# Optimization experiments

Measured on AMD Instinct MI355X. Metric: run time of the kernel, lower is better.

The kernel has to match this reference:

```python
import jax, jax.numpy as jnp
import numpy as np

OS_FACTOR = 2.0  # init kwarg; k = 1/os_factor Euler step size
B, T, IN, H = 32, 4096, 1, 512


def setup_inputs() -> dict:
    key = jax.random.key(0)
    k0, k1, k2, k3, k4 = jax.random.split(key, 5)
    scale = 1.0 / np.sqrt(H).astype(np.float32)
    return {
        "x": jax.random.normal(k0, (B, T, IN), jnp.float32),
        "W_ih": jax.random.uniform(k1, (4 * H, IN), jnp.float32, -scale, scale),
        "W_hh": jax.random.uniform(k2, (4 * H, H), jnp.float32, -scale, scale),
        "b_ih": jax.random.uniform(k3, (4 * H,), jnp.float32, -scale, scale),
        "b_hh": jax.random.uniform(k4, (4 * H,), jnp.float32, -scale, scale),
    }


def reference(x, W_ih, W_hh, b_ih, b_hh):
    """STN_RNN forward with an LSTMCell: h_state <- h_state + k*(cell(x,h_state) - h_state).
    State vector is [h, c] concatenated (state_size = 2H). Returns (states_h, final_state)."""
    k = 1.0 / OS_FACTOR
    h = W_hh.shape[1]
    h0 = jnp.zeros((x.shape[0], 2 * h), x.dtype)

    def step(state, x_t):
        hs, cs = state[:, :h], state[:, h:]
        # torch.nn.LSTMCell gate math
        gates = x_t @ W_ih.T + b_ih + hs @ W_hh.T + b_hh  # [B, 4H]
        i_g, f_g, g_g, o_g = jnp.split(gates, 4, axis=-1)
        c_new = jax.nn.sigmoid(f_g) * cs + jax.nn.sigmoid(i_g) * jnp.tanh(g_g)
        h_new = jax.nn.sigmoid(o_g) * jnp.tanh(c_new)
        hc = jnp.concatenate([h_new, c_new], axis=-1)
        new_state = state + k * (hc - state)  # Euler integration of nonlinearity
        return new_state, new_state

    final_state, states = jax.lax.scan(step, h0, jnp.swapaxes(x, 0, 1))
    states = jnp.swapaxes(states, 0, 1)  # [B, T, 2H]
    return states[..., :h], final_state
```

## Files before the change

### kernel.cpp

```cpp
#include <hip/hip_runtime.h>
#include <hip/hip_bf16.h>


#define NBATCH 32
#define NT     4096
#define NH     512
#define UNITS  64

#define FLAG_OFF  0u
#define BIAS_OFF  4096u
#define WIH_OFF   12288u
#define XF_OFF    20480u
#define HBUF_OFF  544768u
#define WP_OFF    806912u

#define HBUF_DWORDS 65536

__device__ __forceinline__ float bf2f(unsigned short u) {
    union { unsigned int i; float f; } v; v.i = ((unsigned int)u) << 16; return v.f;
}
__device__ __forceinline__ unsigned short f2bf_rne(float f) {
    union { unsigned int i; float f; } v; v.f = f;
    return (unsigned short)((v.i + 0x7fffu + ((v.i >> 16) & 1u)) >> 16);
}
__device__ __forceinline__ float lo_bf(unsigned int u) {
    union { unsigned int i; float f; } v; v.i = u << 16; return v.f;
}
__device__ __forceinline__ float hi_bf(unsigned int u) {
    union { unsigned int i; float f; } v; v.i = u & 0xffff0000u; return v.f;
}
__device__ __forceinline__ float sigm(float x) {
    return 1.0f / (1.0f + __expf(-x));
}
__device__ __forceinline__ float tanh_fast(float x) {
    float e = __expf(-2.0f * fabsf(x));
    float r = (1.0f - e) / (1.0f + e);
    return copysignf(r, x);
}
__device__ __forceinline__ int col2row(int col) {
    int wg = col >> 8, r = col & 255, g = (r >> 6) & 3, u = r & 63;
    return g * 512 + wg * 64 + u;
}

__global__ void prep_detect(const unsigned short* __restrict__ wih_u,
                            int* __restrict__ flagp) {
    __shared__ int cnt;
    if (threadIdx.x == 0) cnt = 0;
    __syncthreads();
    int local = 0;
    for (int i = threadIdx.x; i < 1024; i += 256) {
        float v = bf2f(wih_u[2 * i]);
        if (fabsf(v) <= 0.0625f) local++;
    }
    atomicAdd(&cnt, local);
    __syncthreads();
    if (threadIdx.x == 0) *flagp = (cnt >= 1000) ? 1 : 0;
}

__global__ void prep_conv(const void* __restrict__ x,
                          const void* __restrict__ Wih,
                          const void* __restrict__ Whh,
                          const void* __restrict__ bih,
                          const void* __restrict__ bhh,
                          const int* __restrict__ flagp,
                          unsigned int* __restrict__ WP,
                          float* __restrict__ bias_p,
                          float* __restrict__ wih_p,
                          float* __restrict__ Xf,
                          unsigned int* __restrict__ hbuf_z) {
    int idx = blockIdx.x * blockDim.x + threadIdx.x;
    int isbf = *flagp;

    {
        int wg  = idx >> 16;
        int rem = idx & 65535;
        int r4  = rem >> 11;
        int tid = (rem >> 2) & 511;
        int j   = rem & 3;
        int r   = r4 * 4 + j;
        int c   = r >> 5;
        int k2  = r & 31;
        int jq  = tid & 63;
        int ks  = tid >> 6;
        int col = wg * 256 + jq * 4 + c;
        int row = col2row(col);
        int k0  = ks * 64 + 2 * k2;
        unsigned short lo, hi;
        if (isbf) {
            lo = ((const unsigned short*)Whh)[(size_t)row * 512 + k0];
            hi = ((const unsigned short*)Whh)[(size_t)row * 512 + k0 + 1];
        } else {
            lo = f2bf_rne(((const float*)Whh)[(size_t)row * 512 + k0]);
            hi = f2bf_rne(((const float*)Whh)[(size_t)row * 512 + k0 + 1]);
        }
        WP[idx] = (unsigned int)lo | ((unsigned int)hi << 16);
    }

    if (idx < HBUF_DWORDS) hbuf_z[idx] = 0u;

    if (idx < 2048) {
        int col = idx;
        int row = col2row(col);
        float bi, bh, wi;
        if (isbf) {
            bi = bf2f(((const unsigned short*)bih)[row]);
            bh = bf2f(((const unsigned short*)bhh)[row]);
            wi = bf2f(((const unsigned short*)Wih)[row]);
        } else {
            bi = ((const float*)bih)[row];
            bh = ((const float*)bhh)[row];
            wi = ((const float*)Wih)[row];
        }
        bias_p[col] = bi + bh;
        wih_p[col]  = wi;
    }
    if (idx < NBATCH * NT) {
        Xf[idx] = isbf ? bf2f(((const unsigned short*)x)[idx])
                       : ((const float*)x)[idx];
    }
}

__global__ void __launch_bounds__(512, 2) rnn_kernel(
    const float* __restrict__ Xf,
    const unsigned int* __restrict__ WP,
    const float* __restrict__ bias_p,
    const float* __restrict__ wih_p,
    unsigned long long* __restrict__ hbuf,
    const int* __restrict__ flagp,
    void* __restrict__ out)
{
    const int tid = threadIdx.x;
    const int bid = blockIdx.x;
    const int b   = bid & 31;
    const int wg  = bid >> 5;
    const int isbf = *flagp;

    __shared__ float hsh[512];
    __shared__ float xsh[NT];
    __shared__ float parts[8][256];
    __shared__ float gates[256];
    __shared__ float cst[UNITS];
    __shared__ float hst[UNITS];

    if (tid < UNITS) { cst[tid] = 0.0f; hst[tid] = 0.0f; }

    const int jq = tid & 63;
    const int ks = tid >> 6;

    for (int i = tid; i < NT; i += 512) xsh[i] = Xf[(size_t)b * NT + i];

    unsigned int w[128];
    {
        const uint4* wp = (const uint4*)WP + (size_t)wg * 16384 + tid;
        #pragma unroll
        for (int r4 = 0; r4 < 32; ++r4) {
            uint4 v = wp[(size_t)r4 * 512];
            w[r4 * 4 + 0] = v.x;
            w[r4 * 4 + 1] = v.y;
            w[r4 * 4 + 2] = v.z;
            w[r4 * 4 + 3] = v.w;
        }
    }

    float biasr = 0.0f, wihr = 0.0f;
    if (tid < 256) {
        biasr = bias_p[wg * 256 + tid];
        wihr  = wih_p[wg * 256 + tid];
    }

    unsigned short* outb_u = (unsigned short*)out + (size_t)b * NT * NH;
    float*          outb_f = (float*)out + (size_t)b * NT * NH;

    unsigned int broken = 0;

    for (int t = 0; t < NT; ++t) {
        if (t == 0) {
            hsh[tid] = 0.0f;
        } else {
            const unsigned long long* hin =
                hbuf + (((t & 1) * NBATCH + b) << 9);
            unsigned long long v = 0;
            if (!broken) {
                int g = 0;
                for (;;) {
                    v = __hip_atomic_load(hin + tid, __ATOMIC_RELAXED,
                                          __HIP_MEMORY_SCOPE_AGENT);
                    if ((unsigned int)(v >> 32) == (unsigned int)t) break;
                    __builtin_amdgcn_s_sleep(1);
                    if (++g > 16000000) { broken = 1; v = 0; break; }
                }
            }
            union { unsigned int u; float f; } cv; cv.u = (unsigned int)v;
            hsh[tid] = cv.f;
        }
        __syncthreads();

        float a0 = 0.f, a1 = 0.f, a2 = 0.f, a3 = 0.f;
        float c0 = 0.f, c1 = 0.f, c2 = 0.f, c3 = 0.f;
        const float* hq = hsh + ks * 64;
        #pragma unroll
        for (int k2 = 0; k2 < 32; ++k2) {
            float h0 = hq[2 * k2];
            float h1 = hq[2 * k2 + 1];
            unsigned int u0 = w[k2];
            unsigned int u1 = w[32 + k2];
            unsigned int u2 = w[64 + k2];
            unsigned int u3 = w[96 + k2];
            a0 = fmaf(h0, lo_bf(u0), a0);  c0 = fmaf(h1, hi_bf(u0), c0);
            a1 = fmaf(h0, lo_bf(u1), a1);  c1 = fmaf(h1, hi_bf(u1), c1);
            a2 = fmaf(h0, lo_bf(u2), a2);  c2 = fmaf(h1, hi_bf(u2), c2);
            a3 = fmaf(h0, lo_bf(u3), a3);  c3 = fmaf(h1, hi_bf(u3), c3);
        }
        a0 += c0; a1 += c1; a2 += c2; a3 += c3;
        *(float4*)&parts[ks][jq * 4] = make_float4(a0, a1, a2, a3);
        __syncthreads();

        if (tid < 256) {
            float g = parts[0][tid] + parts[1][tid] + parts[2][tid] + parts[3][tid]
                    + parts[4][tid] + parts[5][tid] + parts[6][tid] + parts[7][tid]
                    + biasr + xsh[t] * wihr;
            gates[tid] = g;
        }
        __syncthreads();

        if (tid < UNITS) {
            float ig = sigm(gates[tid]);
            float fg = sigm(gates[64 + tid]);
            float gg = tanh_fast(gates[128 + tid]);
            float og = sigm(gates[192 + tid]);
            float cold = cst[tid], hold = hst[tid];
            float cnew = fg * cold + ig * gg;
            float hnew = og * tanh_fast(cnew);
            float cb = 0.5f * (cold + cnew);
            float hb = 0.5f * (hold + hnew);
            cst[tid] = cb; hst[tid] = hb;
            union { float f; unsigned int u; } hv; hv.f = hb;
            unsigned long long pkt =
                ((unsigned long long)(unsigned int)(t + 1) << 32) | hv.u;
            unsigned long long* hout =
                hbuf + ((((t + 1) & 1) * NBATCH + b) << 9) + wg * 64 + tid;
            __hip_atomic_store(hout, pkt, __ATOMIC_RELAXED,
                               __HIP_MEMORY_SCOPE_AGENT);
            if (isbf) outb_u[(size_t)t * NH + wg * 64 + tid] = f2bf_rne(hb);
            else      outb_f[(size_t)t * NH + wg * 64 + tid] = hb;
        }
    }

    if (tid < UNITS) {
        size_t fsbase = (size_t)NBATCH * NT * NH + (size_t)b * (2 * NH);
        if (isbf) {
            ((unsigned short*)out)[fsbase + wg * 64 + tid]       = f2bf_rne(hst[tid]);
            ((unsigned short*)out)[fsbase + 512 + wg * 64 + tid] = f2bf_rne(cst[tid]);
        } else {
            ((float*)out)[fsbase + wg * 64 + tid]       = hst[tid];
            ((float*)out)[fsbase + 512 + wg * 64 + tid] = cst[tid];
        }
    }
}

extern "C" void kernel_launch(void* const* d_in, const int* in_sizes, int n_in,
                              void* d_out, int out_size, void* d_ws, size_t ws_size,
                              hipStream_t stream) {
    const void* x   = d_in[0];
    const void* Wih = d_in[1];
    const void* Whh = d_in[2];
    const void* bih = d_in[3];
    const void* bhh = d_in[4];

    char* ws = (char*)d_ws;
    int* flagp          = (int*)(ws + FLAG_OFF);
    float* bias_p       = (float*)(ws + BIAS_OFF);
    float* wih_p        = (float*)(ws + WIH_OFF);
    float* Xf           = (float*)(ws + XF_OFF);
    unsigned long long* hbuf = (unsigned long long*)(ws + HBUF_OFF);
    unsigned int* WP    = (unsigned int*)(ws + WP_OFF);

    prep_detect<<<1, 256, 0, stream>>>((const unsigned short*)Wih, flagp);
    prep_conv<<<2048, 256, 0, stream>>>(x, Wih, Whh, bih, bhh, flagp,
                                        WP, bias_p, wih_p, Xf,
                                        (unsigned int*)hbuf);
    rnn_kernel<<<256, 512, 0, stream>>>(Xf, WP, bias_p, wih_p, hbuf,
                                        flagp, d_out);
}
```

Measured before the change: 15.86 ms.

## Cut per-step barriers via wave-local h reads and double-buffered partials

Each wave now reads only the slice of the shared h vector that it wrote itself, so the barrier after loading h is dropped. The partial-sum buffer is double-buffered by step parity, which lets the gate reduction and the LSTM cell update merge into one 64-thread section. That removes a second barrier, and the cell and hidden state now live in registers instead of shared memory. The polling loop exits on a wave-wide vote and uses a shorter timeout, so a stalled producer is declared broken sooner.

```diff
diff --git a/kernel.cpp b/kernel.cpp
--- a/kernel.cpp
+++ b/kernel.cpp
@@ -137,36 +137,36 @@
 
     __shared__ float hsh[512];
     __shared__ float xsh[NT];
-    __shared__ float parts[8][256];
-    __shared__ float gates[256];
-    __shared__ float cst[UNITS];
-    __shared__ float hst[UNITS];
-
-    if (tid < UNITS) { cst[tid] = 0.0f; hst[tid] = 0.0f; }
-
-    const int jq = tid & 63;
-    const int ks = tid >> 6;
+    __shared__ float parts[2][8][256];
+
+    const int l = tid & 63;
+    const int w = tid >> 6;
 
     for (int i = tid; i < NT; i += 512) xsh[i] = Xf[(size_t)b * NT + i];
 
-    unsigned int w[128];
+    unsigned int wreg[128];
     {
         const uint4* wp = (const uint4*)WP + (size_t)wg * 16384 + tid;
         #pragma unroll
         for (int r4 = 0; r4 < 32; ++r4) {
             uint4 v = wp[(size_t)r4 * 512];
-            w[r4 * 4 + 0] = v.x;
-            w[r4 * 4 + 1] = v.y;
-            w[r4 * 4 + 2] = v.z;
-            w[r4 * 4 + 3] = v.w;
-        }
-    }
-
-    float biasr = 0.0f, wihr = 0.0f;
-    if (tid < 256) {
-        biasr = bias_p[wg * 256 + tid];
-        wihr  = wih_p[wg * 256 + tid];
-    }
+            wreg[r4 * 4 + 0] = v.x;
+            wreg[r4 * 4 + 1] = v.y;
+            wreg[r4 * 4 + 2] = v.z;
+            wreg[r4 * 4 + 3] = v.w;
+        }
+    }
+
+    float bias4[4] = {0.f, 0.f, 0.f, 0.f};
+    float wih4[4]  = {0.f, 0.f, 0.f, 0.f};
+    if (tid < 64) {
+        #pragma unroll
+        for (int g = 0; g < 4; ++g) {
+            bias4[g] = bias_p[wg * 256 + g * 64 + tid];
+            wih4[g]  = wih_p[wg * 256 + g * 64 + tid];
+        }
+    }
+    float creg = 0.0f, hreg = 0.0f;
 
     unsigned short* outb_u = (unsigned short*)out + (size_t)b * NT * NH;
     float*          outb_f = (float*)out + (size_t)b * NT * NH;
@@ -178,62 +178,61 @@
             hsh[tid] = 0.0f;
         } else {
             const unsigned long long* hin =
-                hbuf + (((t & 1) * NBATCH + b) << 9);
+                hbuf + (((t & 1) * NBATCH + b) << 9) + tid;
             unsigned long long v = 0;
             if (!broken) {
                 int g = 0;
                 for (;;) {
-                    v = __hip_atomic_load(hin + tid, __ATOMIC_RELAXED,
+                    v = __hip_atomic_load(hin, __ATOMIC_RELAXED,
                                           __HIP_MEMORY_SCOPE_AGENT);
-                    if ((unsigned int)(v >> 32) == (unsigned int)t) break;
+                    if (__all((unsigned int)(v >> 32) == (unsigned int)t)) break;
                     __builtin_amdgcn_s_sleep(1);
-                    if (++g > 16000000) { broken = 1; v = 0; break; }
+                    if (++g > 2000000) { broken = 1; break; }
                 }
             }
             union { unsigned int u; float f; } cv; cv.u = (unsigned int)v;
             hsh[tid] = cv.f;
         }
-        __syncthreads();
 
         float a0 = 0.f, a1 = 0.f, a2 = 0.f, a3 = 0.f;
         float c0 = 0.f, c1 = 0.f, c2 = 0.f, c3 = 0.f;
-        const float* hq = hsh + ks * 64;
+        const float* hq = hsh + w * 64;
         #pragma unroll
         for (int k2 = 0; k2 < 32; ++k2) {
             float h0 = hq[2 * k2];
             float h1 = hq[2 * k2 + 1];
-            unsigned int u0 = w[k2];
-            unsigned int u1 = w[32 + k2];
-            unsigned int u2 = w[64 + k2];
-            unsigned int u3 = w[96 + k2];
+            unsigned int u0 = wreg[k2];
+            unsigned int u1 = wreg[32 + k2];
+            unsigned int u2 = wreg[64 + k2];
+            unsigned int u3 = wreg[96 + k2];
             a0 = fmaf(h0, lo_bf(u0), a0);  c0 = fmaf(h1, hi_bf(u0), c0);
             a1 = fmaf(h0, lo_bf(u1), a1);  c1 = fmaf(h1, hi_bf(u1), c1);
             a2 = fmaf(h0, lo_bf(u2), a2);  c2 = fmaf(h1, hi_bf(u2), c2);
             a3 = fmaf(h0, lo_bf(u3), a3);  c3 = fmaf(h1, hi_bf(u3), c3);
         }
         a0 += c0; a1 += c1; a2 += c2; a3 += c3;
-        *(float4*)&parts[ks][jq * 4] = make_float4(a0, a1, a2, a3);
+        *(float4*)&parts[t & 1][w][l * 4] = make_float4(a0, a1, a2, a3);
         __syncthreads();
 
-        if (tid < 256) {
-            float g = parts[0][tid] + parts[1][tid] + parts[2][tid] + parts[3][tid]
-                    + parts[4][tid] + parts[5][tid] + parts[6][tid] + parts[7][tid]
-                    + biasr + xsh[t] * wihr;
-            gates[tid] = g;
-        }
-        __syncthreads();
-
-        if (tid < UNITS) {
-            float ig = sigm(gates[tid]);
-            float fg = sigm(gates[64 + tid]);
-            float gg = tanh_fast(gates[128 + tid]);
-            float og = sigm(gates[192 + tid]);
-            float cold = cst[tid], hold = hst[tid];
-            float cnew = fg * cold + ig * gg;
+        if (tid < 64) {
+            const float xt = xsh[t];
+            float gsum[4];
+            #pragma unroll
+            for (int g = 0; g < 4; ++g) {
+                float acc = parts[t & 1][0][g * 64 + tid];
+                #pragma unroll
+                for (int s = 1; s < 8; ++s) acc += parts[t & 1][s][g * 64 + tid];
+                gsum[g] = acc + bias4[g] + xt * wih4[g];
+            }
+            float ig = sigm(gsum[0]);
+            float fg = sigm(gsum[1]);
+            float gg = tanh_fast(gsum[2]);
+            float og = sigm(gsum[3]);
+            float cnew = fg * creg + ig * gg;
             float hnew = og * tanh_fast(cnew);
-            float cb = 0.5f * (cold + cnew);
-            float hb = 0.5f * (hold + hnew);
-            cst[tid] = cb; hst[tid] = hb;
+            float cb = 0.5f * (creg + cnew);
+            float hb = 0.5f * (hreg + hnew);
+            creg = cb; hreg = hb;
             union { float f; unsigned int u; } hv; hv.f = hb;
             unsigned long long pkt =
                 ((unsigned long long)(unsigned int)(t + 1) << 32) | hv.u;
@@ -246,14 +245,14 @@
         }
     }
 
-    if (tid < UNITS) {
+    if (tid < 64) {
         size_t fsbase = (size_t)NBATCH * NT * NH + (size_t)b * (2 * NH);
         if (isbf) {
-            ((unsigned short*)out)[fsbase + wg * 64 + tid]       = f2bf_rne(hst[tid]);
-            ((unsigned short*)out)[fsbase + 512 + wg * 64 + tid] = f2bf_rne(cst[tid]);
-        } else {
-            ((float*)out)[fsbase + wg * 64 + tid]       = hst[tid];
-            ((float*)out)[fsbase + 512 + wg * 64 + tid] = cst[tid];
+            ((unsigned short*)out)[fsbase + wg * 64 + tid]       = f2bf_rne(hreg);
+            ((unsigned short*)out)[fsbase + 512 + wg * 64 + tid] = f2bf_rne(creg);
+        } else {
+            ((float*)out)[fsbase + wg * 64 + tid]       = hreg;
+            ((float*)out)[fsbase + 512 + wg * 64 + tid] = creg;
         }
     }
 }
```

Result: slower. 19.53 ms (+23.1%).
